# Optimization experiments

Hardware: AMD Instinct MI355X
Metric: run time of the kernel (lower is better)

Reference implementation:

```python
import jax, jax.numpy as jnp
import numpy as np


def setup_inputs() -> dict:
    key = jax.random.key(0)
    k1, k2 = jax.random.split(key)
    B, DIM, T, SIZE = 64, 512, 2048, 1024
    H = jax.random.normal(k1, (B, DIM, T), dtype=jnp.float32)
    units = jax.random.normal(k2, (DIM, SIZE), dtype=jnp.float32)
    return {"H": H, "units": units}


def reference(H, units):
    # H: (B, dim, T), units: (dim, size)
    # Original: C[b, s, t] = exp(-||H[b,:,t] - units[:,s]||^2) normalized over s.
    # exp(-d^2) / sum_s exp(-d^2) == softmax(-d^2, axis=s).
    Ht = jnp.swapaxes(H, 1, 2)                      # (B, T, dim)
    h_sq = jnp.sum(Ht * Ht, axis=-1, keepdims=True)  # (B, T, 1)
    m_sq = jnp.sum(units * units, axis=0)            # (size,)
    cross = jnp.einsum('btd,ds->bts', Ht, units)     # (B, T, size) GEMM
    sqdist = h_sq - 2.0 * cross + m_sq               # (B, T, size)
    C = jax.nn.softmax(-sqdist, axis=-1)             # normalize over codebook
    return jnp.swapaxes(C, 1, 2)                     # (B, size, T)
```

## Files before the change

### kernel.cpp

```cpp
#include <hip/hip_runtime.h>
#include <stdint.h>


typedef unsigned short u16;
typedef __attribute__((ext_vector_type(8))) short short8;
typedef __attribute__((ext_vector_type(4))) float f32x4;
typedef __attribute__((ext_vector_type(16))) float f32x16;

#define B_DIM 64
#define DIM   512
#define T_DIM 2048
#define S_DIM 1024

__device__ __forceinline__ u16 f32_to_bf16(float f) {
  uint32_t u = __float_as_uint(f);
  uint32_t r = u + 0x7FFFu + ((u >> 16) & 1u);
  return (u16)(r >> 16);
}
__device__ __forceinline__ float bf16_to_f32(u16 h) {
  return __uint_as_float(((uint32_t)h) << 16);
}

__global__ __launch_bounds__(256) void k_prep_units(const float* __restrict__ units,
                                                    u16* __restrict__ UpH, u16* __restrict__ UpL,
                                                    float* __restrict__ msq) {
  const int s0 = blockIdx.x * 4;
  const int tid = threadIdx.x;
  const int lane = tid & 63, wv = tid >> 6;
  float acc0 = 0.f, acc1 = 0.f, acc2 = 0.f, acc3 = 0.f;
#pragma unroll
  for (int j = 0; j < 2; ++j) {
    const int d = tid + j * 256;
    const float4 v = *(const float4*)(units + (size_t)d * S_DIM + s0);
    acc0 += v.x * v.x; acc1 += v.y * v.y; acc2 += v.z * v.z; acc3 += v.w * v.w;
    const int dbase = (d >> 4) * 16384 + ((d >> 3) & 1) * 256 + (d & 7);
    const float fv[4] = {v.x, v.y, v.z, v.w};
#pragma unroll
    for (int q = 0; q < 4; ++q) {
      const int s = s0 + q;
      const int idx = dbase + ((s >> 5) * 64 + (s & 31)) * 8;
      const u16 h = f32_to_bf16(fv[q]);
      UpH[idx] = h;
      UpL[idx] = f32_to_bf16(fv[q] - bf16_to_f32(h));
    }
  }
#pragma unroll
  for (int off = 1; off < 64; off <<= 1) {
    acc0 += __shfl_xor(acc0, off);
    acc1 += __shfl_xor(acc1, off);
    acc2 += __shfl_xor(acc2, off);
    acc3 += __shfl_xor(acc3, off);
  }
  __shared__ float part[4][4];
  if (lane == 0) { part[wv][0] = acc0; part[wv][1] = acc1; part[wv][2] = acc2; part[wv][3] = acc3; }
  __syncthreads();
  if (tid < 4) msq[s0 + tid] = part[0][tid] + part[1][tid] + part[2][tid] + part[3][tid];
}

__global__ __launch_bounds__(256) void k_prep_h(const float* __restrict__ H,
                                                u16* __restrict__ BpH, u16* __restrict__ BpL) {
  __shared__ float tile[64 * 68];
  const int bx = blockIdx.x;
  const int d0 = blockIdx.y * 64;
  const int b = blockIdx.z;
  const int t0 = bx * 64;
  const int tid = threadIdx.x;
#pragma unroll
  for (int j = 0; j < 4; ++j) {
    const int chunk = tid + j * 256;
    const int r = chunk >> 4, c4 = (chunk & 15) * 4;
    const float4 v = *(const float4*)(H + ((size_t)(b * DIM + d0 + r)) * T_DIM + t0 + c4);
    *(float4*)(&tile[r * 68 + c4]) = v;
  }
  __syncthreads();
#pragma unroll
  for (int j = 0; j < 2; ++j) {
    const int chunk = tid + j * 256;
    const int q = chunk >> 3, e8 = (chunk & 7) * 8;
    union { u16 us[8]; uint4 v4; } hi, lo;
#pragma unroll
    for (int k = 0; k < 8; ++k) {
      const float f = tile[(e8 + k) * 68 + q];
      const u16 h = f32_to_bf16(f);
      hi.us[k] = h;
      lo.us[k] = f32_to_bf16(f - bf16_to_f32(h));
    }
    const int dg = d0 + e8;
    const int chunkB = (q >> 5) * 64 + ((dg >> 3) & 1) * 32 + (q & 31);
    const size_t o = ((((size_t)b * 32 + bx) * 32 + (dg >> 4)) * 128 + chunkB) * 8;
    *(uint4*)(BpH + o) = hi.v4;
    *(uint4*)(BpL + o) = lo.v4;
  }
}

__global__ __launch_bounds__(512, 2) void k_fused(const u16* __restrict__ UpH, const u16* __restrict__ UpL,
                                                  const u16* __restrict__ BpH, const u16* __restrict__ BpL,
                                                  const float* __restrict__ msq,
                                                  float* __restrict__ out) {
  __shared__ float redM[8][64];
  __shared__ float redS[8][64];
  const int tid = threadIdx.x;
  const int lane = tid & 63, wv = tid >> 6;
  const int l31 = lane & 31, lhi = lane >> 5;
  const int sw = wv;

  const int tgx = blockIdx.x;
  const int t00 = tgx * 64;
  const int bb = blockIdx.y;

  const char* const aH = (const char*)UpH + (sw * 4) * 1024 + lane * 16;
  const char* const aL = (const char*)UpL + (sw * 4) * 1024 + lane * 16;
  const size_t bg = (((size_t)bb * 32 + tgx) * 32) * 2048 + lane * 16;
  const char* const bH = (const char*)BpH + bg;
  const char* const bL = (const char*)BpL + bg;

  f32x16 acc[4][2];
#pragma unroll
  for (int mt = 0; mt < 4; ++mt)
#pragma unroll
    for (int nt = 0; nt < 2; ++nt)
#pragma unroll
      for (int r = 0; r < 16; ++r)
        acc[mt][nt][r] = 0.f;

  short8 ahA[4], ahB[4];
  short8 bhA[2], bhB[2];
  short8 al[4];
  short8 bl[2];

#define LD_AH(D, KS) do { const size_t ko = (size_t)(KS) * 32768;            \
    (D)[0] = *(const short8*)(aH + ko);                                      \
    (D)[1] = *(const short8*)(aH + ko + 1024);                               \
    (D)[2] = *(const short8*)(aH + ko + 2048);                               \
    (D)[3] = *(const short8*)(aH + ko + 3072); } while (0)
#define LD_AL(D, KS) do { const size_t ko = (size_t)(KS) * 32768;            \
    (D)[0] = *(const short8*)(aL + ko);                                      \
    (D)[1] = *(const short8*)(aL + ko + 1024);                               \
    (D)[2] = *(const short8*)(aL + ko + 2048);                               \
    (D)[3] = *(const short8*)(aL + ko + 3072); } while (0)
#define LD_BH(D, KS) do { const size_t ko = (size_t)(KS) * 2048;             \
    (D)[0] = *(const short8*)(bH + ko);                                      \
    (D)[1] = *(const short8*)(bH + ko + 1024); } while (0)
#define LD_BL(D, KS) do { const size_t ko = (size_t)(KS) * 2048;             \
    (D)[0] = *(const short8*)(bL + ko);                                      \
    (D)[1] = *(const short8*)(bL + ko + 1024); } while (0)

#define MM8(AF, BF)                                                          \
    __builtin_amdgcn_s_setprio(1);                                           \
    _Pragma("unroll") for (int mt = 0; mt < 4; ++mt)                         \
      _Pragma("unroll") for (int nt = 0; nt < 2; ++nt)                       \
        acc[mt][nt] = __builtin_amdgcn_mfma_f32_32x32x16_bf16((AF)[mt], (BF)[nt], acc[mt][nt], 0, 0, 0); \
    __builtin_amdgcn_s_setprio(0);

  LD_AH(ahA, 0); LD_BH(bhA, 0); LD_BL(bl, 0); LD_AL(al, 0);
  LD_AH(ahB, 1); LD_BH(bhB, 1);

#pragma unroll 1
  for (int k = 0; k < 32; k += 2) {
    const int kc2 = (k + 2 < 32) ? (k + 2) : 30;
    const int kc3 = (k + 3 < 32) ? (k + 3) : 31;
    MM8(ahA, bhA);
    MM8(ahA, bl);
    LD_BL(bl, k + 1);
    LD_AH(ahA, kc2);
    MM8(al, bhA);
    LD_AL(al, k + 1);
    LD_BH(bhA, kc2);
    MM8(ahB, bhB);
    MM8(ahB, bl);
    LD_BL(bl, kc2);
    LD_AH(ahB, kc3);
    MM8(al, bhB);
    LD_AL(al, kc2);
    LD_BH(bhB, kc3);
  }

  float mx0 = -3.0e38f, mx1 = -3.0e38f;
#pragma unroll
  for (int mt = 0; mt < 4; ++mt) {
    const int sb = sw * 128 + mt * 32 + lhi * 4;
#pragma unroll
    for (int q = 0; q < 4; ++q) {
      const f32x4 mq = *(const f32x4*)(msq + sb + q * 8);
#pragma unroll
      for (int r = 0; r < 4; ++r) {
        const int reg = q * 4 + r;
        const float v0 = 2.f * acc[mt][0][reg] - mq[r];
        const float v1 = 2.f * acc[mt][1][reg] - mq[r];
        acc[mt][0][reg] = v0; acc[mt][1][reg] = v1;
        mx0 = fmaxf(mx0, v0); mx1 = fmaxf(mx1, v1);
      }
    }
  }
  mx0 = fmaxf(mx0, __shfl_xor(mx0, 32));
  mx1 = fmaxf(mx1, __shfl_xor(mx1, 32));
  if (lane < 32) { redM[wv][l31] = mx0; redM[wv][32 + l31] = mx1; }
  __syncthreads();
  float M0 = redM[0][l31], M1 = redM[0][32 + l31];
#pragma unroll
  for (int w = 1; w < 8; ++w) {
    M0 = fmaxf(M0, redM[w][l31]);
    M1 = fmaxf(M1, redM[w][32 + l31]);
  }
  float s0 = 0.f, s1 = 0.f;
#pragma unroll
  for (int mt = 0; mt < 4; ++mt)
#pragma unroll
    for (int reg = 0; reg < 16; ++reg) {
      const float e0 = __expf(acc[mt][0][reg] - M0);
      const float e1 = __expf(acc[mt][1][reg] - M1);
      acc[mt][0][reg] = e0; acc[mt][1][reg] = e1;
      s0 += e0; s1 += e1;
    }
  s0 += __shfl_xor(s0, 32);
  s1 += __shfl_xor(s1, 32);
  if (lane < 32) { redS[wv][l31] = s0; redS[wv][32 + l31] = s1; }
  __syncthreads();
  float S0 = redS[0][l31], S1 = redS[0][32 + l31];
#pragma unroll
  for (int w = 1; w < 8; ++w) {
    S0 += redS[w][l31];
    S1 += redS[w][32 + l31];
  }
  const float r0 = 1.0f / S0, r1 = 1.0f / S1;

  float* const outb = out + ((size_t)bb << 21);
  const int tc0 = t00 + l31, tc1 = t00 + 32 + l31;
#pragma unroll
  for (int mt = 0; mt < 4; ++mt) {
    const int sb = sw * 128 + mt * 32 + lhi * 4;
#pragma unroll
    for (int q = 0; q < 4; ++q)
#pragma unroll
      for (int r = 0; r < 4; ++r) {
        const int srow = sb + q * 8 + r;
        const int reg = q * 4 + r;
        outb[(size_t)srow * T_DIM + tc0] = acc[mt][0][reg] * r0;
        outb[(size_t)srow * T_DIM + tc1] = acc[mt][1][reg] * r1;
      }
  }
}

extern "C" void kernel_launch(void* const* d_in, const int* in_sizes, int n_in,
                              void* d_out, int out_size, void* d_ws, size_t ws_size,
                              hipStream_t stream) {
  (void)in_sizes; (void)n_in; (void)out_size; (void)ws_size;
  const float* H = (const float*)d_in[0];
  const float* units = (const float*)d_in[1];
  float* out = (float*)d_out;
  char* ws = (char*)d_ws;
  u16* BpH = (u16*)(ws);
  u16* BpL = (u16*)(ws + 134217728);
  u16* UpH = (u16*)(ws + 268435456);
  u16* UpL = (u16*)(ws + 269484032);
  float* msq = (float*)(ws + 270532608);

  k_prep_units<<<dim3(S_DIM / 4), 256, 0, stream>>>(units, UpH, UpL, msq);
  k_prep_h<<<dim3(T_DIM / 64, DIM / 64, B_DIM), 256, 0, stream>>>(H, BpH, BpL);
  k_fused<<<dim3(T_DIM / 64, B_DIM), 512, 0, stream>>>(UpH, UpL, BpH, BpL, msq, out);
}
```

Before: 572.3 us.

## Stage B operand tile in LDS via async global_load_lds shared across waves

All eight waves previously loaded the same B (H-derived) fragments directly from global memory into registers. Now the block's whole B tile, both hi and lo halves, is staged into a 132 KB shared buffer with direct-to-LDS global loads: half up front, the rest spread over the first loop iterations, with one barrier at k==10. The main loop is also restructured into two independent register sets per k-step, with B fragments read from LDS. This removes redundant global/L2 traffic for B, but the large LDS footprint may cap occupancy below the two blocks per CU the launch bounds request.

New measurement: 577.8 us. About the same (+1.0%).

```diff
diff --git a/kernel.cpp b/kernel.cpp
--- a/kernel.cpp
+++ b/kernel.cpp
@@ -11,6 +11,11 @@
 #define DIM   512
 #define T_DIM 2048
 #define S_DIM 1024
+
+#define B_LO_O 65536
+#define REDM_O 131072
+#define REDS_O 133120
+#define SM_SZ  135168
 
 __device__ __forceinline__ u16 f32_to_bf16(float f) {
   uint32_t u = __float_as_uint(f);
@@ -93,12 +98,19 @@
   }
 }
 
+__device__ __forceinline__ void gl16(const void* g, void* l) {
+  __builtin_amdgcn_global_load_lds((const __attribute__((address_space(1))) void*)g,
+                                   (__attribute__((address_space(3))) void*)l, 16, 0, 0);
+}
+
+#define WAITV0() asm volatile("s_waitcnt vmcnt(0)" ::: "memory")
+#define SYNCPT() do { __builtin_amdgcn_s_barrier(); __builtin_amdgcn_sched_barrier(0); } while (0)
+
 __global__ __launch_bounds__(512, 2) void k_fused(const u16* __restrict__ UpH, const u16* __restrict__ UpL,
                                                   const u16* __restrict__ BpH, const u16* __restrict__ BpL,
                                                   const float* __restrict__ msq,
                                                   float* __restrict__ out) {
-  __shared__ float redM[8][64];
-  __shared__ float redS[8][64];
+  __shared__ __align__(16) char sm[SM_SZ];
   const int tid = threadIdx.x;
   const int lane = tid & 63, wv = tid >> 6;
   const int l31 = lane & 31, lhi = lane >> 5;
@@ -110,9 +122,9 @@
 
   const char* const aH = (const char*)UpH + (sw * 4) * 1024 + lane * 16;
   const char* const aL = (const char*)UpL + (sw * 4) * 1024 + lane * 16;
-  const size_t bg = (((size_t)bb * 32 + tgx) * 32) * 2048 + lane * 16;
-  const char* const bH = (const char*)BpH + bg;
-  const char* const bL = (const char*)BpL + bg;
+  const size_t bgBase = (((size_t)bb * 32 + tgx) * 32) * 2048;
+  const char* const pBH = (const char*)BpH + bgBase;
+  const char* const pBL = (const char*)BpL + bgBase;
 
   f32x16 acc[4][2];
 #pragma unroll
@@ -123,10 +135,8 @@
       for (int r = 0; r < 16; ++r)
         acc[mt][nt][r] = 0.f;
 
-  short8 ahA[4], ahB[4];
-  short8 bhA[2], bhB[2];
-  short8 al[4];
-  short8 bl[2];
+  short8 ah0[4], ah1[4], al0[4], al1[4];
+  short8 bh0[2], bh1[2], bl0[2], bl1[2];
 
 #define LD_AH(D, KS) do { const size_t ko = (size_t)(KS) * 32768;            \
     (D)[0] = *(const short8*)(aH + ko);                                      \
@@ -138,12 +148,14 @@
     (D)[1] = *(const short8*)(aL + ko + 1024);                               \
     (D)[2] = *(const short8*)(aL + ko + 2048);                               \
     (D)[3] = *(const short8*)(aL + ko + 3072); } while (0)
-#define LD_BH(D, KS) do { const size_t ko = (size_t)(KS) * 2048;             \
-    (D)[0] = *(const short8*)(bH + ko);                                      \
-    (D)[1] = *(const short8*)(bH + ko + 1024); } while (0)
-#define LD_BL(D, KS) do { const size_t ko = (size_t)(KS) * 2048;             \
-    (D)[0] = *(const short8*)(bL + ko);                                      \
-    (D)[1] = *(const short8*)(bL + ko + 1024); } while (0)
+#define DS_B(BH, BL, KS) do { const int bo = (KS) * 2048 + lane * 16;        \
+    (BH)[0] = *(const short8*)(sm + bo);                                     \
+    (BH)[1] = *(const short8*)(sm + bo + 1024);                              \
+    (BL)[0] = *(const short8*)(sm + B_LO_O + bo);                            \
+    (BL)[1] = *(const short8*)(sm + B_LO_O + bo + 1024); } while (0)
+#define STG(J) do { const int off = (16 + 2 * (J)) * 2048 + (wv & 3) * 1024 + lane * 16; \
+    if (wv < 4) gl16(pBH + off, sm + off);                                   \
+    else        gl16(pBL + off, sm + B_LO_O + off); } while (0)
 
 #define MM8(AF, BF)                                                          \
     __builtin_amdgcn_s_setprio(1);                                           \
@@ -152,29 +164,38 @@
         acc[mt][nt] = __builtin_amdgcn_mfma_f32_32x32x16_bf16((AF)[mt], (BF)[nt], acc[mt][nt], 0, 0, 0); \
     __builtin_amdgcn_s_setprio(0);
 
-  LD_AH(ahA, 0); LD_BH(bhA, 0); LD_BL(bl, 0); LD_AL(al, 0);
-  LD_AH(ahB, 1); LD_BH(bhB, 1);
+#pragma unroll
+  for (int r = 0; r < 4; ++r) {
+    const int off = (tid + r * 512) * 16;
+    gl16(pBH + off, sm + off);
+    gl16(pBL + off, sm + B_LO_O + off);
+  }
+  LD_AH(ah0, 0); LD_AL(al0, 0);
+  WAITV0();
+  SYNCPT();
+  DS_B(bh0, bl0, 0);
+  LD_AH(ah1, 1); LD_AL(al1, 1);
+  DS_B(bh1, bl1, 1);
 
 #pragma unroll 1
   for (int k = 0; k < 32; k += 2) {
-    const int kc2 = (k + 2 < 32) ? (k + 2) : 30;
+    if (k == 10) { WAITV0(); SYNCPT(); }
+    const int kc2 = (k + 2 < 32) ? (k + 2) : 31;
     const int kc3 = (k + 3 < 32) ? (k + 3) : 31;
-    MM8(ahA, bhA);
-    MM8(ahA, bl);
-    LD_BL(bl, k + 1);
-    LD_AH(ahA, kc2);
-    MM8(al, bhA);
-    LD_AL(al, k + 1);
-    LD_BH(bhA, kc2);
-    MM8(ahB, bhB);
-    MM8(ahB, bl);
-    LD_BL(bl, kc2);
-    LD_AH(ahB, kc3);
-    MM8(al, bhB);
-    LD_AL(al, kc2);
-    LD_BH(bhB, kc3);
-  }
-
+    if (k < 8) STG(k);
+    MM8(ah0, bh0);
+    MM8(ah0, bl0);
+    MM8(al0, bh0);
+    LD_AH(ah0, kc2); LD_AL(al0, kc2); DS_B(bh0, bl0, kc2);
+    if (k + 1 < 8) STG(k + 1);
+    MM8(ah1, bh1);
+    MM8(ah1, bl1);
+    MM8(al1, bh1);
+    LD_AH(ah1, kc3); LD_AL(al1, kc3); DS_B(bh1, bl1, kc3);
+  }
+
+  float* redM = (float*)(sm + REDM_O);
+  float* redS = (float*)(sm + REDS_O);
   float mx0 = -3.0e38f, mx1 = -3.0e38f;
 #pragma unroll
   for (int mt = 0; mt < 4; ++mt) {
@@ -194,13 +215,13 @@
   }
   mx0 = fmaxf(mx0, __shfl_xor(mx0, 32));
   mx1 = fmaxf(mx1, __shfl_xor(mx1, 32));
-  if (lane < 32) { redM[wv][l31] = mx0; redM[wv][32 + l31] = mx1; }
-  __syncthreads();
-  float M0 = redM[0][l31], M1 = redM[0][32 + l31];
+  if (lane < 32) { redM[wv * 64 + l31] = mx0; redM[wv * 64 + 32 + l31] = mx1; }
+  __syncthreads();
+  float M0 = redM[l31], M1 = redM[32 + l31];
 #pragma unroll
   for (int w = 1; w < 8; ++w) {
-    M0 = fmaxf(M0, redM[w][l31]);
-    M1 = fmaxf(M1, redM[w][32 + l31]);
+    M0 = fmaxf(M0, redM[w * 64 + l31]);
+    M1 = fmaxf(M1, redM[w * 64 + 32 + l31]);
   }
   float s0 = 0.f, s1 = 0.f;
 #pragma unroll
@@ -214,13 +235,13 @@
     }
   s0 += __shfl_xor(s0, 32);
   s1 += __shfl_xor(s1, 32);
-  if (lane < 32) { redS[wv][l31] = s0; redS[wv][32 + l31] = s1; }
-  __syncthreads();
-  float S0 = redS[0][l31], S1 = redS[0][32 + l31];
+  if (lane < 32) { redS[wv * 64 + l31] = s0; redS[wv * 64 + 32 + l31] = s1; }
+  __syncthreads();
+  float S0 = redS[l31], S1 = redS[32 + l31];
 #pragma unroll
   for (int w = 1; w < 8; ++w) {
-    S0 += redS[w][l31];
-    S1 += redS[w][32 + l31];
+    S0 += redS[w * 64 + l31];
+    S1 += redS[w * 64 + 32 + l31];
   }
   const float r0 = 1.0f / S0, r1 = 1.0f / S1;
 
```
